# Kernel tuning notes

Measured on AMD Instinct MI355X. Metric: run time of the kernel, lower is better.

Reference implementation:

```python
import jax, jax.numpy as jnp
import numpy as np

N = 128  # padded Hadamard size (find_min_power(122))
H1 = W1 = 122

def _hadamard(n):
    H = np.array([[1.0]], dtype=np.float32)
    while H.shape[0] < n:
        H = np.block([[H, H], [H, -H]])
    return H

_H = jnp.asarray(_hadamard(N))  # symmetric 128x128 +/-1 matrix
_DN = ('NCHW', 'OIHW', 'NCHW')

def _conv(x, w, b, stride, pad):
    y = jax.lax.conv_general_dilated(x, w, (stride, stride),
                                     [(pad, pad), (pad, pad)], dimension_numbers=_DN)
    return y + b[None, :, None, None]

def _convT(x, w, b, stride, pad):
    # torch ConvTranspose2d weight layout [in, out, kh, kw]
    k = w.shape[-1]
    wf = jnp.flip(w, (2, 3)).transpose(1, 0, 2, 3)  # -> [out, in, kh, kw]
    p = k - 1 - pad
    y = jax.lax.conv_general_dilated(x, wf, (1, 1), [(p, p), (p, p)],
                                     lhs_dilation=(stride, stride), dimension_numbers=_DN)
    return y + b[None, :, None, None]

def _fwht2(x):
    # fwht along -1 then -2 (dense Hadamard matmul, matching fast=False path)
    x = jnp.einsum('bchw,wk->bchk', x, _H)
    return jnp.einsum('bchw,hk->bckw', x, _H)

def _ifwht2(x):
    x = jnp.einsum('bchw,wk->bchk', x, _H) / N
    return jnp.einsum('bchw,hk->bckw', x, _H) / N

def _pad(x):
    return jnp.pad(x, ((0, 0), (0, 0), (0, N - H1), (0, N - W1)))

def _thresh(x, T):
    aT = jnp.abs(T)
    s = jnp.copysign(jax.nn.relu(jnp.abs(x) - aT), x)
    return s + jnp.sign(s) * aT

def _kl(q):
    e = q.size // 64
    p = jax.nn.sigmoid(jnp.full((64,), 0.001, q.dtype))
    qm = jnp.sum(jax.nn.sigmoid(jnp.abs(q).reshape(e, 64)), axis=0) / e
    return jnp.sum(p * jnp.log(p / qm)) + jnp.sum((1 - p) * jnp.log((1 - p) / (1 - qm)))

def _tv(x, weight):
    b, c, h, w = x.shape
    tv = jnp.abs(x[:, :, 1:, :] - x[:, :, :-1, :]).sum() + \
         jnp.abs(x[:, :, :, 1:] - x[:, :, :, :-1]).sum()
    return weight * tv / (b * c * h * w)

def setup_inputs() -> dict:
    key = jax.random.key(0)
    ks = jax.random.split(key, 16)
    B = 128
    inp = {
        'x': jax.random.normal(ks[0], (B, 1, 256, 256), jnp.float32),
        'val': 0,
        'v1': jax.random.uniform(ks[1], (N, N), jnp.float32),
        'T1': jax.random.uniform(ks[2], (N, N), jnp.float32) / 10,
        'v2': jax.random.uniform(ks[3], (N, N), jnp.float32),
        'T2': jax.random.uniform(ks[4], (N, N), jnp.float32) / 10,
        'v3': jax.random.uniform(ks[5], (N, N), jnp.float32),
        'T3': jax.random.uniform(ks[6], (N, N), jnp.float32) / 10,
        'w1': jax.random.normal(ks[7], (4, 1, 16, 16), jnp.float32) * 0.05,
        'b1': jax.random.normal(ks[8], (4,), jnp.float32) * 0.01,
        'w2': jax.random.normal(ks[9], (4, 4, 7, 7), jnp.float32) * 0.05,
        'b2': jax.random.normal(ks[10], (4,), jnp.float32) * 0.01,
        'w3': jax.random.normal(ks[11], (4, 4, 7, 7), jnp.float32) * 0.05,  # [in,out,kh,kw]
        'b3': jax.random.normal(ks[12], (4,), jnp.float32) * 0.01,
        'w4': jax.random.normal(ks[13], (4, 1, 16, 16), jnp.float32) * 0.05,  # [in,out,kh,kw]
        'b4': jax.random.normal(ks[14], (1,), jnp.float32) * 0.01,
    }
    return inp

def reference(x, val, v1, T1, v2, T2, v3, T3, w1, b1, w2, b2, w3, b3, w4, b4):
    TV_WEIGHT = 0.05  # original draws np.random.uniform(0, 0.1); fixed for determinism
    x1 = _conv(x, w1, b1, 2, 1)                       # [B,4,122,122]
    x6 = _thresh(v1 * _fwht2(_pad(x1)), T1)           # [B,4,128,128]
    x9 = _ifwht2(x6)[..., :H1, :W1]
    x10 = _conv(x9, w2, b2, 1, 3)                     # [B,4,122,122]
    x15 = _thresh(v2 * _fwht2(_pad(x10)), T2)
    x18 = _ifwht2(x15)[..., :H1, :W1]
    x19 = _convT(x18, w3, b3, 1, 3) + x10
    x24 = _thresh(v3 * _fwht2(_pad(x19)), T3)
    x27 = _ifwht2(x24 + x6)[..., :H1, :W1]
    out = _convT(x27, w4, b4, 2, 1) * x               # [B,1,256,256]
    loss = 1.0 * _tv(out, TV_WEIGHT) + 0.1 * (_kl(x6) + _kl(x15) + _kl(x24))
    return out, loss
```

## Files before the change

### kernel.cpp

```cpp
#include <hip/hip_runtime.h>
#include <math.h>

#define PLANE 16384
#define NPLANES 512

typedef __attribute__((ext_vector_type(2))) unsigned int uint2v;

__device__ __forceinline__ void fwht2d_reg512(float* __restrict__ v, float* __restrict__ xch,
                                              int W, int L) {
#pragma unroll
    for (int m = 1; m <= 2; m <<= 1) {
#pragma unroll
        for (int r = 0; r < 32; ++r) {
            if (!(r & m)) {
                int s = r | m;
                float a = v[r], b = v[s];
                v[r] = a + b; v[s] = a - b;
            }
        }
    }
    {
        float sg = (L & 1) ? -1.f : 1.f;
#pragma unroll
        for (int r = 0; r < 32; ++r) {
            int xi = __float_as_int(v[r]);
            float p = __int_as_float(__builtin_amdgcn_update_dpp(xi, xi, 0xB1, 0xF, 0xF, false));
            v[r] = fmaf(sg, v[r], p);
        }
    }
    {
        float sg = (L & 2) ? -1.f : 1.f;
#pragma unroll
        for (int r = 0; r < 32; ++r) {
            int xi = __float_as_int(v[r]);
            float p = __int_as_float(__builtin_amdgcn_update_dpp(xi, xi, 0x4E, 0xF, 0xF, false));
            v[r] = fmaf(sg, v[r], p);
        }
    }
    {
        float sg = (L & 4) ? -1.f : 1.f;
#pragma unroll
        for (int r = 0; r < 32; ++r) {
            float p = __shfl_xor(v[r], 4);
            v[r] = fmaf(sg, v[r], p);
        }
    }
    {
        float sg = (L & 8) ? -1.f : 1.f;
#pragma unroll
        for (int r = 0; r < 32; ++r) {
            int xi = __float_as_int(v[r]);
            float p = __int_as_float(__builtin_amdgcn_update_dpp(xi, xi, 0x128, 0xF, 0xF, false));
            v[r] = fmaf(sg, v[r], p);
        }
    }
#pragma unroll
    for (int r = 0; r < 32; r += 2) {
        uint2v s1 = __builtin_amdgcn_permlane16_swap(__float_as_uint(v[r]),
                                                     __float_as_uint(v[r + 1]), false, false);
        float u = __uint_as_float(s1.x) + __uint_as_float(s1.y);
        float w = __uint_as_float(s1.x) - __uint_as_float(s1.y);
        uint2v s2 = __builtin_amdgcn_permlane16_swap(__float_as_uint(u),
                                                     __float_as_uint(w), false, false);
        v[r]     = __uint_as_float(s2.x);
        v[r + 1] = __uint_as_float(s2.y);
    }
#pragma unroll
    for (int r = 0; r < 32; r += 2) {
        uint2v s1 = __builtin_amdgcn_permlane32_swap(__float_as_uint(v[r]),
                                                     __float_as_uint(v[r + 1]), false, false);
        float u = __uint_as_float(s1.x) + __uint_as_float(s1.y);
        float w = __uint_as_float(s1.x) - __uint_as_float(s1.y);
        uint2v s2 = __builtin_amdgcn_permlane32_swap(__float_as_uint(u),
                                                     __float_as_uint(w), false, false);
        v[r]     = __uint_as_float(s2.x);
        v[r + 1] = __uint_as_float(s2.y);
    }
#pragma unroll
    for (int m = 4; m <= 16; m <<= 1) {
#pragma unroll
        for (int r = 0; r < 32; ++r) {
            if (!(r & m)) {
                int s = r | m;
                float a = v[r], b = v[s];
                v[r] = a + b; v[s] = a - b;
            }
        }
    }
#pragma unroll
    for (int mw = 1; mw <= 4; mw <<= 1) {
        int Wp = W ^ mw;
        float sg = (W & mw) ? -1.f : 1.f;
#pragma unroll
        for (int half = 0; half < 2; ++half) {
            __syncthreads();
#pragma unroll
            for (int j = 0; j < 16; ++j)
                xch[(j * 8 + W) * 64 + L] = v[half * 16 + j];
            __syncthreads();
#pragma unroll
            for (int j = 0; j < 16; ++j) {
                float p = xch[(j * 8 + Wp) * 64 + L];
                v[half * 16 + j] = fmaf(sg, v[half * 16 + j], p);
            }
        }
    }
}

template <bool ADDPOST>
__global__ __launch_bounds__(512) void fwht_kernel_t(
    const float* __restrict__ in, const float* __restrict__ vmat,
    const float* __restrict__ tmat, const float* __restrict__ addbuf,
    float* __restrict__ outInv, float* __restrict__ klpart)
{
    __shared__ float xch[16 * 512];
    const int tid = threadIdx.x;
    const int W = tid >> 6, L = tid & 63;
    const int plane = blockIdx.x;
    const int hbase = W * 16 + ((L >> 5) << 3);
    const int wbase = (L & 31) << 2;
    const float* src = in + (size_t)plane * PLANE;

    float v[32];
#pragma unroll
    for (int g = 0; g < 8; ++g) {
        float4 t = *(const float4*)&src[(hbase + g) * 128 + wbase];
        v[4 * g] = t.x; v[4 * g + 1] = t.y; v[4 * g + 2] = t.z; v[4 * g + 3] = t.w;
    }

    fwht2d_reg512(v, xch, W, L);

    float ls0 = 0.f, ls1 = 0.f, ls2 = 0.f, ls3 = 0.f;
#pragma unroll
    for (int g = 0; g < 8; ++g) {
        int rowoff = (hbase + g) * 128 + wbase;
        float4 vm = *(const float4*)&vmat[rowoff];
        float4 tm = *(const float4*)&tmat[rowoff];
        float y0 = v[4 * g]     * vm.x;
        float y1 = v[4 * g + 1] * vm.y;
        float y2 = v[4 * g + 2] * vm.z;
        float y3 = v[4 * g + 3] * vm.w;
        y0 = (fabsf(y0) > fabsf(tm.x)) ? y0 : 0.f;
        y1 = (fabsf(y1) > fabsf(tm.y)) ? y1 : 0.f;
        y2 = (fabsf(y2) > fabsf(tm.z)) ? y2 : 0.f;
        y3 = (fabsf(y3) > fabsf(tm.w)) ? y3 : 0.f;
        ls0 += 1.f / (1.f + __expf(-fabsf(y0)));
        ls1 += 1.f / (1.f + __expf(-fabsf(y1)));
        ls2 += 1.f / (1.f + __expf(-fabsf(y2)));
        ls3 += 1.f / (1.f + __expf(-fabsf(y3)));
        v[4 * g] = y0; v[4 * g + 1] = y1; v[4 * g + 2] = y2; v[4 * g + 3] = y3;
    }
#pragma unroll
    for (int m = 16; m <= 32; m <<= 1) {
        ls0 += __shfl_xor(ls0, m);
        ls1 += __shfl_xor(ls1, m);
        ls2 += __shfl_xor(ls2, m);
        ls3 += __shfl_xor(ls3, m);
    }
    if (L < 16) {
        float4 o; o.x = ls0; o.y = ls1; o.z = ls2; o.w = ls3;
        *(float4*)&klpart[(size_t)(plane * 8 + W) * 64 + 4 * L] = o;
    }

    fwht2d_reg512(v, xch, W, L);

    float* dst = outInv + (size_t)plane * PLANE;
    const float s = 1.f / 16384.f;
#pragma unroll
    for (int g = 0; g < 8; ++g) {
        int h = hbase + g;
        int rowoff = h * 128 + wbase;
        bool rv = h < 122;
        float4 ad = make_float4(0.f, 0.f, 0.f, 0.f);
        if (ADDPOST) ad = *(const float4*)&addbuf[(size_t)plane * PLANE + rowoff];
        float4 o;
        o.x = (rv && wbase + 0 < 122) ? fmaf(v[4 * g],     s, ad.x) : 0.f;
        o.y = (rv && wbase + 1 < 122) ? fmaf(v[4 * g + 1], s, ad.y) : 0.f;
        o.z = (rv && wbase + 2 < 122) ? fmaf(v[4 * g + 2], s, ad.z) : 0.f;
        o.w = (rv && wbase + 3 < 122) ? fmaf(v[4 * g + 3], s, ad.w) : 0.f;
        *(float4*)&dst[rowoff] = o;
    }
}

__global__ void prep_weights(const float* __restrict__ w3, const float* __restrict__ w4,
                             float* __restrict__ w3c, float* __restrict__ w4p)
{
    int tid = blockIdx.x * 256 + threadIdx.x;
    if (tid < 784) {
        int oc = tid / 196;
        int rem = tid - oc * 196;
        int ic = rem / 49;
        int k = rem - ic * 49;
        int kh = k / 7, kw = k - kh * 7;
        w3c[(oc * 4 + ic) * 49 + k] = w3[(ic * 4 + oc) * 49 + (6 - kh) * 7 + (6 - kw)];
    }
    if (tid < 1024) {
        int u = tid & 7, t = (tid >> 3) & 7, pb = (tid >> 6) & 1, pa = (tid >> 7) & 1, ic = tid >> 8;
        int kh = 2 * t + (pa ? 0 : 1);
        int kw = 2 * u + (pb ? 0 : 1);
        w4p[tid] = w4[ic * 256 + kh * 16 + kw];
    }
}

__global__ __launch_bounds__(256) void conv1_kernel(
    const float* __restrict__ x, const float* __restrict__ w1,
    const float* __restrict__ b1, float* __restrict__ out)
{
    __shared__ float tile[2][78][44];
    int tx = blockIdx.x, ty = blockIdx.y, b = blockIdx.z;
    int tid = threadIdx.x;
    const float* xp = x + (size_t)b * 65536;
    int r0g = ty * 64 - 1, c0g = tx * 64 - 1;
    for (int i = tid; i < 78 * 78; i += 256) {
        int rr = i / 78, cc = i - rr * 78;
        int gi = r0g + rr, gj = c0g + cc;
        float v = (gi >= 0 && gi < 256 && gj >= 0 && gj < 256) ? xp[gi * 256 + gj] : 0.f;
        tile[cc & 1][rr][cc >> 1] = v;
    }
    __syncthreads();
    int cg = tid & 7, r = tid >> 3;
    int B = cg * 4;
    float acc[4][4];
#pragma unroll
    for (int oc = 0; oc < 4; ++oc)
#pragma unroll
        for (int c = 0; c < 4; ++c) acc[oc][c] = 0.f;
#pragma unroll 1
    for (int kh = 0; kh < 16; ++kh) {
        float win[2][12];
        const float* te = &tile[0][2 * r + kh][B];
        const float* to = &tile[1][2 * r + kh][B];
#pragma unroll
        for (int k = 0; k < 3; ++k) {
            *(float4*)&win[0][4 * k] = *(const float4*)&te[4 * k];
            *(float4*)&win[1][4 * k] = *(const float4*)&to[4 * k];
        }
#pragma unroll
        for (int oc = 0; oc < 4; ++oc) {
            const float* wr = w1 + oc * 256 + kh * 16;
#pragma unroll
            for (int kw = 0; kw < 16; ++kw) {
                float wv = wr[kw];
                const float* wp8 = win[kw & 1];
                int q = kw >> 1;
#pragma unroll
                for (int c = 0; c < 4; ++c)
                    acc[oc][c] = fmaf(wp8[c + q], wv, acc[oc][c]);
            }
        }
    }
    int oh = ty * 32 + r;
    int owb = tx * 32 + B;
    bool rowv = oh < 122;
#pragma unroll
    for (int oc = 0; oc < 4; ++oc) {
        float bv = b1[oc];
        float4 res;
        res.x = (rowv && owb + 0 < 122) ? acc[oc][0] + bv : 0.f;
        res.y = (rowv && owb + 1 < 122) ? acc[oc][1] + bv : 0.f;
        res.z = (rowv && owb + 2 < 122) ? acc[oc][2] + bv : 0.f;
        res.w = (rowv && owb + 3 < 122) ? acc[oc][3] + bv : 0.f;
        *(float4*)&out[(((size_t)b * 4 + oc) << 14) + (oh << 7) + owb] = res;
    }
}

__global__ __launch_bounds__(256) void conv7_kernel(
    const float* __restrict__ in, const float* __restrict__ w,
    const float* __restrict__ bias, const float* __restrict__ skip,
    float* __restrict__ out)
{
    __shared__ float tile[4][38][40];
    int tx = blockIdx.x, ty = blockIdx.y, b = blockIdx.z;
    int tid = threadIdx.x;
    int r0g = ty * 32 - 3, c0g = tx * 32 - 3;
    for (int i = tid; i < 4 * 38 * 38; i += 256) {
        int ic = i / 1444;
        int rem = i - ic * 1444;
        int rr = rem / 38, cc = rem - rr * 38;
        int gi = r0g + rr, gj = c0g + cc;
        float v = 0.f;
        if (gi >= 0 && gi < 128 && gj >= 0 && gj < 128)
            v = in[(((size_t)b * 4 + ic) << 14) + (gi << 7) + gj];
        tile[ic][rr][cc] = v;
    }
    __syncthreads();
    int cg = tid & 7, r = tid >> 3;
    int B = cg * 4;
    float acc[4][4];
#pragma unroll
    for (int oc = 0; oc < 4; ++oc)
#pragma unroll
        for (int c = 0; c < 4; ++c) acc[oc][c] = 0.f;
#pragma unroll 1
    for (int ic = 0; ic < 4; ++ic) {
#pragma unroll 1
        for (int kh = 0; kh < 7; ++kh) {
            float win[12];
            const float* trow = &tile[ic][r + kh][B];
#pragma unroll
            for (int k = 0; k < 3; ++k)
                *(float4*)&win[4 * k] = *(const float4*)&trow[4 * k];
#pragma unroll
            for (int oc = 0; oc < 4; ++oc) {
                const float* wr = w + (oc * 4 + ic) * 49 + kh * 7;
#pragma unroll
                for (int kw = 0; kw < 7; ++kw) {
                    float wv = wr[kw];
#pragma unroll
                    for (int c = 0; c < 4; ++c)
                        acc[oc][c] = fmaf(win[c + kw], wv, acc[oc][c]);
                }
            }
        }
    }
    int oh = ty * 32 + r;
    int owb = tx * 32 + B;
    bool rowv = oh < 122;
#pragma unroll
    for (int oc = 0; oc < 4; ++oc) {
        size_t o = (((size_t)b * 4 + oc) << 14) + (oh << 7) + owb;
        float4 sv = make_float4(0.f, 0.f, 0.f, 0.f);
        if (skip) sv = *(const float4*)&skip[o];
        float bv = bias[oc];
        float4 res;
        res.x = (rowv && owb + 0 < 122) ? acc[oc][0] + bv + sv.x : 0.f;
        res.y = (rowv && owb + 1 < 122) ? acc[oc][1] + bv + sv.y : 0.f;
        res.z = (rowv && owb + 2 < 122) ? acc[oc][2] + bv + sv.z : 0.f;
        res.w = (rowv && owb + 3 < 122) ? acc[oc][3] + bv + sv.w : 0.f;
        *(float4*)&out[o] = res;
    }
}

#define CT_HALF(T, ROW, PA)                                                    \
    _Pragma("unroll")                                                          \
    for (int pb = 0; pb < 2; ++pb) {                                           \
        const float* w8 = wp + (((ic * 2 + (PA)) * 2 + pb) * 8 + (T)) * 8;     \
        _Pragma("unroll")                                                      \
        for (int u = 0; u < 8; ++u) {                                          \
            float wv = w8[u];                                                  \
            _Pragma("unroll")                                                  \
            for (int c = 0; c < 4; ++c)                                        \
                acc[PA][pb][c] = fmaf(ROW[8 + c + pb - u], wv, acc[PA][pb][c]);\
        }                                                                      \
    }

#define LOADROW(BUF, R)                                                        \
    _Pragma("unroll")                                                          \
    for (int k = 0; k < 4; ++k)                                                \
        *(float4*)&BUF[4 * k] = *(const float4*)&tld[(R) * 44 + 4 * cg + 4 * k];

__global__ __launch_bounds__(256) void convt4_kernel(
    const float* __restrict__ in, const float* __restrict__ wp,
    const float* __restrict__ bias, const float* __restrict__ xin,
    float* __restrict__ out)
{
    __shared__ float tile[2][40][44];
    int tx = blockIdx.x, ty = blockIdx.y, b = blockIdx.z;
    int tid = threadIdx.x;
    int A0 = ty * 32, B0 = tx * 32;
    int r0g = A0 - 7, c0g = B0 - 8;
    int cg = tid & 7, ra = tid >> 3;
    float acc[2][2][4];
#pragma unroll
    for (int pa = 0; pa < 2; ++pa)
#pragma unroll
        for (int pb = 0; pb < 2; ++pb)
#pragma unroll
            for (int c = 0; c < 4; ++c) acc[pa][pb][c] = 0.f;

#pragma unroll 1
    for (int icp = 0; icp < 2; ++icp) {
        __syncthreads();
        for (int i = tid; i < 2 * 40 * 44; i += 256) {
            int ics = i / 1760;
            int rem = i - ics * 1760;
            int rr = rem / 44, cc = rem - rr * 44;
            int gi = r0g + rr, gj = c0g + cc;
            int icg = icp * 2 + ics;
            float v = 0.f;
            if (gi >= 0 && gi < 128 && gj >= 0 && gj < 128)
                v = in[(((size_t)b * 4 + icg) << 14) + (gi << 7) + gj];
            tile[ics][rr][cc] = v;
        }
        __syncthreads();
#pragma unroll 1
        for (int ics = 0; ics < 2; ++ics) {
            const int ic = icp * 2 + ics;
            const float* tld = &tile[ics][0][0];
            float bufA[16], bufB[16];
            LOADROW(bufB, ra + 8)
#pragma unroll 1
            for (int t2 = 0; t2 < 8; t2 += 2) {
                LOADROW(bufA, ra + 7 - t2)
                CT_HALF(t2, bufA, 0)
                CT_HALF(t2, bufB, 1)
                LOADROW(bufB, ra + 6 - t2)
                CT_HALF(t2 + 1, bufB, 0)
                CT_HALF(t2 + 1, bufA, 1)
            }
        }
    }
    int oh0 = 2 * (A0 + ra);
    int owb = 2 * (B0 + 4 * cg);
    float bv = bias[0];
#pragma unroll
    for (int pa = 0; pa < 2; ++pa) {
        size_t o = (size_t)b * 65536 + (size_t)(oh0 + pa) * 256 + owb;
        float4 x0 = *(const float4*)&xin[o];
        float4 x1 = *(const float4*)&xin[o + 4];
        float4 r0, r1;
        r0.x = (acc[pa][0][0] + bv) * x0.x;
        r0.y = (acc[pa][1][0] + bv) * x0.y;
        r0.z = (acc[pa][0][1] + bv) * x0.z;
        r0.w = (acc[pa][1][1] + bv) * x0.w;
        r1.x = (acc[pa][0][2] + bv) * x1.x;
        r1.y = (acc[pa][1][2] + bv) * x1.y;
        r1.z = (acc[pa][0][3] + bv) * x1.z;
        r1.w = (acc[pa][1][3] + bv) * x1.w;
        *(float4*)&out[o] = r0;
        *(float4*)&out[o + 4] = r1;
    }
}

__global__ __launch_bounds__(256) void tv_kernel(
    const float* __restrict__ out, float* __restrict__ tvpart)
{
    const float4* out4 = (const float4*)out;
    __shared__ float red[256];
    int tid = threadIdx.x;
    float local = 0.f;
    const int total4 = 128 * 65536 / 4;
    for (int i4 = blockIdx.x * 256 + tid; i4 < total4; i4 += gridDim.x * 256) {
        float4 a = out4[i4];
        int i = i4 << 2;
        local += fabsf(a.y - a.x) + fabsf(a.z - a.y) + fabsf(a.w - a.z);
        if ((i & 255) != 252) local += fabsf(out[i + 4] - a.w);
        if ((i & 65535) < 65280) {
            float4 c = out4[i4 + 64];
            local += fabsf(c.x - a.x) + fabsf(c.y - a.y) + fabsf(c.z - a.z) + fabsf(c.w - a.w);
        }
    }
    red[tid] = local;
    __syncthreads();
    for (int s = 128; s > 0; s >>= 1) {
        if (tid < s) red[tid] += red[tid + s];
        __syncthreads();
    }
    if (tid == 0) tvpart[blockIdx.x] = red[0];
}

__global__ __launch_bounds__(256) void reduce1_kernel(
    const float* __restrict__ klpart, const float* __restrict__ tvpart,
    float* __restrict__ klred, float* __restrict__ tvred)
{
    int bid = blockIdx.x;
    int tid = threadIdx.x;
    if (bid < 48) {
        int layer = bid >> 4, chunk = bid & 15;
        int sub = tid >> 6, t = tid & 63;
        const float* base = klpart + (size_t)layer * 262144 + (size_t)chunk * 256 * 64;
        float s = 0.f;
        for (int r = sub; r < 256; r += 4)
            s += base[r * 64 + t];
        __shared__ float red[4][64];
        red[sub][t] = s;
        __syncthreads();
        if (tid < 64)
            klred[(layer * 16 + chunk) * 64 + tid] =
                red[0][tid] + red[1][tid] + red[2][tid] + red[3][tid];
    } else {
        __shared__ float red[256];
        float s = 0.f;
        for (int i = tid; i < 2048; i += 256) s += tvpart[i];
        red[tid] = s;
        __syncthreads();
        for (int st = 128; st > 0; st >>= 1) {
            if (tid < st) red[tid] += red[tid + st];
            __syncthreads();
        }
        if (tid == 0) tvred[0] = red[0];
    }
}

__global__ __launch_bounds__(64) void finalize2_kernel(
    const float* __restrict__ klred, const float* __restrict__ tvred,
    float* __restrict__ lossout)
{
    int t = threadIdx.x;
    float p = 1.f / (1.f + __expf(-0.001f));
    float term = 0.f;
#pragma unroll
    for (int l = 0; l < 3; ++l) {
        float q = 0.f;
#pragma unroll
        for (int c = 0; c < 16; ++c)
            q += klred[(l * 16 + c) * 64 + t];
        float qm = q * (1.f / 131072.f);
        term += p * logf(p / qm) + (1.f - p) * logf((1.f - p) / (1.f - qm));
    }
#pragma unroll
    for (int off = 32; off > 0; off >>= 1)
        term += __shfl_down(term, off);
    if (t == 0)
        lossout[0] = 0.05f * tvred[0] / 8388608.f + 0.1f * term;
}

extern "C" void kernel_launch(void* const* d_in, const int* in_sizes, int n_in,
                              void* d_out, int out_size, void* d_ws, size_t ws_size,
                              hipStream_t stream) {
    (void)in_sizes; (void)n_in; (void)out_size; (void)ws_size;
    const float* x  = (const float*)d_in[0];
    const float* v1 = (const float*)d_in[2];
    const float* T1 = (const float*)d_in[3];
    const float* v2 = (const float*)d_in[4];
    const float* T2 = (const float*)d_in[5];
    const float* v3 = (const float*)d_in[6];
    const float* T3 = (const float*)d_in[7];
    const float* w1 = (const float*)d_in[8];
    const float* b1 = (const float*)d_in[9];
    const float* w2 = (const float*)d_in[10];
    const float* b2 = (const float*)d_in[11];
    const float* w3 = (const float*)d_in[12];
    const float* b3 = (const float*)d_in[13];
    const float* w4 = (const float*)d_in[14];
    const float* b4 = (const float*)d_in[15];
    float* out = (float*)d_out;

    float* W0 = (float*)d_ws;
    float* W1 = W0 + (size_t)NPLANES * PLANE;
    float* W2 = W1 + (size_t)NPLANES * PLANE;
    float* klpart = W2 + (size_t)NPLANES * PLANE;
    float* tvpart = klpart + 3 * 4096 * 64;
    float* klred  = tvpart + 2048;
    float* tvred  = klred + 3072;
    float* w3c = tvred + 64;
    float* w4p = w3c + 784;
    float* x10buf = out;

    prep_weights<<<4, 256, 0, stream>>>(w3, w4, w3c, w4p);
    conv1_kernel<<<dim3(4, 4, 128), 256, 0, stream>>>(x, w1, b1, W0);
    fwht_kernel_t<false><<<NPLANES, 512, 0, stream>>>(W0, v1, T1, nullptr, W1, klpart);
    conv7_kernel<<<dim3(4, 4, 128), 256, 0, stream>>>(W1, w2, b2, nullptr, x10buf);
    fwht_kernel_t<false><<<NPLANES, 512, 0, stream>>>(x10buf, v2, T2, nullptr, W0, klpart + 262144);
    conv7_kernel<<<dim3(4, 4, 128), 256, 0, stream>>>(W0, w3c, b3, x10buf, W2);
    fwht_kernel_t<true><<<NPLANES, 512, 0, stream>>>(W2, v3, T3, W1, W0, klpart + 2 * 262144);
    convt4_kernel<<<dim3(4, 4, 128), 256, 0, stream>>>(W0, w4p, b4, x, out);
    tv_kernel<<<2048, 256, 0, stream>>>(out, tvpart);
    reduce1_kernel<<<49, 256, 0, stream>>>(klpart, tvpart, klred, tvred);
    finalize2_kernel<<<1, 64, 0, stream>>>(klred, tvred, out + 8388608);
}
```

Before: 354.4 us.

## Fuse total-variation loss into transposed-conv epilogue and handle tile seams in reducer

The separate TV kernel, which re-read the whole 32 MB output, is removed. Each convt4 block now stages its 64x64 output tile in shared memory and computes the in-tile TV differences, writing one partial per block. The differences that cross tile borders (rows and columns 63/64, 127/128, 191/192) are computed by 8 extra blocks added to reduce1. This saves one full pass over global memory and a kernel launch, at the cost of extra shared-memory traffic and syncs in the convt epilogue, plus scattered seam reads.

```diff
diff --git a/kernel.cpp b/kernel.cpp
--- a/kernel.cpp
+++ b/kernel.cpp
@@ -352,9 +352,10 @@
 __global__ __launch_bounds__(256) void convt4_kernel(
     const float* __restrict__ in, const float* __restrict__ wp,
     const float* __restrict__ bias, const float* __restrict__ xin,
-    float* __restrict__ out)
-{
-    __shared__ float tile[2][40][44];
+    float* __restrict__ out, float* __restrict__ tvpart)
+{
+    __shared__ float sbuf[4224];
+    float (*tile)[40][44] = (float(*)[40][44])sbuf;
     int tx = blockIdx.x, ty = blockIdx.y, b = blockIdx.z;
     int tid = threadIdx.x;
     int A0 = ty * 32, B0 = tx * 32;
@@ -403,6 +404,7 @@
     int oh0 = 2 * (A0 + ra);
     int owb = 2 * (B0 + 4 * cg);
     float bv = bias[0];
+    float4 res[2][2];
 #pragma unroll
     for (int pa = 0; pa < 2; ++pa) {
         size_t o = (size_t)b * 65536 + (size_t)(oh0 + pa) * 256 + owb;
@@ -419,38 +421,43 @@
         r1.w = (acc[pa][1][3] + bv) * x1.w;
         *(float4*)&out[o] = r0;
         *(float4*)&out[o + 4] = r1;
-    }
-}
-
-__global__ __launch_bounds__(256) void tv_kernel(
-    const float* __restrict__ out, float* __restrict__ tvpart)
-{
-    const float4* out4 = (const float4*)out;
-    __shared__ float red[256];
-    int tid = threadIdx.x;
+        res[pa][0] = r0; res[pa][1] = r1;
+    }
+
+    __syncthreads();
+    int lr0 = 2 * ra, lc = 8 * cg;
+#pragma unroll
+    for (int pa = 0; pa < 2; ++pa) {
+        *(float4*)&sbuf[(lr0 + pa) * 66 + lc]     = res[pa][0];
+        *(float4*)&sbuf[(lr0 + pa) * 66 + lc + 4] = res[pa][1];
+    }
+    __syncthreads();
     float local = 0.f;
-    const int total4 = 128 * 65536 / 4;
-    for (int i4 = blockIdx.x * 256 + tid; i4 < total4; i4 += gridDim.x * 256) {
-        float4 a = out4[i4];
-        int i = i4 << 2;
+#pragma unroll 1
+    for (int i = tid; i < 1024; i += 256) {
+        int rr = i >> 4, c4 = (i & 15) << 2;
+        float4 a = *(const float4*)&sbuf[rr * 66 + c4];
         local += fabsf(a.y - a.x) + fabsf(a.z - a.y) + fabsf(a.w - a.z);
-        if ((i & 255) != 252) local += fabsf(out[i + 4] - a.w);
-        if ((i & 65535) < 65280) {
-            float4 c = out4[i4 + 64];
-            local += fabsf(c.x - a.x) + fabsf(c.y - a.y) + fabsf(c.z - a.z) + fabsf(c.w - a.w);
-        }
-    }
-    red[tid] = local;
+        if (c4 < 60) local += fabsf(sbuf[rr * 66 + c4 + 4] - a.w);
+        if (rr < 63) {
+            float4 d = *(const float4*)&sbuf[(rr + 1) * 66 + c4];
+            local += fabsf(d.x - a.x) + fabsf(d.y - a.y) + fabsf(d.z - a.z) + fabsf(d.w - a.w);
+        }
+    }
+#pragma unroll
+    for (int off = 32; off > 0; off >>= 1) local += __shfl_down(local, off);
     __syncthreads();
-    for (int s = 128; s > 0; s >>= 1) {
-        if (tid < s) red[tid] += red[tid + s];
-        __syncthreads();
-    }
-    if (tid == 0) tvpart[blockIdx.x] = red[0];
+    if ((tid & 63) == 0) sbuf[tid >> 6] = local;
+    __syncthreads();
+    if (tid == 0) {
+        int bid = (b * 4 + ty) * 4 + tx;
+        tvpart[bid] = sbuf[0] + sbuf[1] + sbuf[2] + sbuf[3];
+    }
 }
 
 __global__ __launch_bounds__(256) void reduce1_kernel(
     const float* __restrict__ klpart, const float* __restrict__ tvpart,
+    const float* __restrict__ out,
     float* __restrict__ klred, float* __restrict__ tvred)
 {
     int bid = blockIdx.x;
@@ -468,7 +475,7 @@
         if (tid < 64)
             klred[(layer * 16 + chunk) * 64 + tid] =
                 red[0][tid] + red[1][tid] + red[2][tid] + red[3][tid];
-    } else {
+    } else if (bid == 48) {
         __shared__ float red[256];
         float s = 0.f;
         for (int i = tid; i < 2048; i += 256) s += tvpart[i];
@@ -479,6 +486,33 @@
             __syncthreads();
         }
         if (tid == 0) tvred[0] = red[0];
+    } else {
+        int blockn = bid - 49;
+        __shared__ float red[256];
+        float s = 0.f;
+        for (int p = blockn * 24576 + tid; p < (blockn + 1) * 24576; p += 256) {
+            if (p < 98304) {
+                int j = p >> 15, rem = p & 32767;
+                int b = rem >> 8, k = rem & 255;
+                int h = 63 + 64 * j;
+                size_t o = (size_t)b * 65536 + (size_t)h * 256 + k;
+                s += fabsf(out[o + 256] - out[o]);
+            } else {
+                int q = p - 98304;
+                int j = q >> 15, rem = q & 32767;
+                int b = rem >> 8, h = rem & 255;
+                int w = 63 + 64 * j;
+                size_t o = (size_t)b * 65536 + (size_t)h * 256 + w;
+                s += fabsf(out[o + 1] - out[o]);
+            }
+        }
+        red[tid] = s;
+        __syncthreads();
+        for (int st = 128; st > 0; st >>= 1) {
+            if (tid < st) red[tid] += red[tid + st];
+            __syncthreads();
+        }
+        if (tid == 0) tvred[1 + blockn] = red[0];
     }
 }
 
@@ -501,8 +535,12 @@
 #pragma unroll
     for (int off = 32; off > 0; off >>= 1)
         term += __shfl_down(term, off);
-    if (t == 0)
-        lossout[0] = 0.05f * tvred[0] / 8388608.f + 0.1f * term;
+    if (t == 0) {
+        float tv = 0.f;
+#pragma unroll
+        for (int i = 0; i < 9; ++i) tv += tvred[i];
+        lossout[0] = 0.05f * tv / 8388608.f + 0.1f * term;
+    }
 }
 
 extern "C" void kernel_launch(void* const* d_in, const int* in_sizes, int n_in,
@@ -533,7 +571,7 @@
     float* tvpart = klpart + 3 * 4096 * 64;
     float* klred  = tvpart + 2048;
     float* tvred  = klred + 3072;
-    float* w3c = tvred + 64;
+    float* w3c = tvred + 16;
     float* w4p = w3c + 784;
     float* x10buf = out;
 
@@ -544,8 +582,7 @@
     fwht_kernel_t<false><<<NPLANES, 512, 0, stream>>>(x10buf, v2, T2, nullptr, W0, klpart + 262144);
     conv7_kernel<<<dim3(4, 4, 128), 256, 0, stream>>>(W0, w3c, b3, x10buf, W2);
     fwht_kernel_t<true><<<NPLANES, 512, 0, stream>>>(W2, v3, T3, W1, W0, klpart + 2 * 262144);
-    convt4_kernel<<<dim3(4, 4, 128), 256, 0, stream>>>(W0, w4p, b4, x, out);
-    tv_kernel<<<2048, 256, 0, stream>>>(out, tvpart);
-    reduce1_kernel<<<49, 256, 0, stream>>>(klpart, tvpart, klred, tvred);
+    convt4_kernel<<<dim3(4, 4, 128), 256, 0, stream>>>(W0, w4p, b4, x, out, tvpart);
+    reduce1_kernel<<<57, 256, 0, stream>>>(klpart, tvpart, out, klred, tvred);
     finalize2_kernel<<<1, 64, 0, stream>>>(klred, tvred, out + 8388608);
 }
```

Result: slower. 396.0 us (+11.7%).
